# Kernel tuning notes

Measured on AMD Instinct MI355X. Metric: run time of the kernel, lower is better.

Reference implementation:

```python
import jax, jax.numpy as jnp
import numpy as np

B, N_NODES, VOCAB, H = 128, 1023, 2048, 256  # depth-9 perfect binary trees (heap layout)


def setup_inputs() -> dict:
    key = jax.random.key(0)
    k1, k2, k3, k4, k5 = jax.random.split(key, 5)
    tokens = jax.random.randint(k1, (B, N_NODES), 0, VOCAB)
    emb = jax.random.normal(k2, (VOCAB, H), dtype=jnp.float32) * 0.02
    Wx = jax.random.normal(k3, (H, 5 * H), dtype=jnp.float32) * 0.02
    Ul = jax.random.normal(k4, (H, 5 * H), dtype=jnp.float32) * 0.02
    Ur = jax.random.normal(k5, (H, 5 * H), dtype=jnp.float32) * 0.02
    b = jnp.zeros((5 * H,), dtype=jnp.float32)
    return {"tokens": tokens, "emb": emb, "Wx": Wx, "Ul": Ul, "Ur": Ur, "b": b}


def _tree_lstm(tokens, emb, Wx, Ul, Ur, b):
    # tokens: [B, 2^(D+1)-1] in level-order heap layout; children of heap index i
    # are 2i+1, 2i+2 -> within level d+1 they sit at offsets 2k, 2k+1.
    n_nodes = tokens.shape[1]
    depth = int(np.log2(n_nodes + 1)) - 1
    hdim = emb.shape[1]
    x_all = emb[tokens]  # [B, N, H] embedding lookup (memory-bound gather)
    h = c = None
    for d in range(depth, -1, -1):  # bottom-up over levels (fixed structural loop)
        start, n = 2 ** d - 1, 2 ** d
        x = x_all[:, start:start + n]  # [B, n, H]
        gates = jnp.einsum('bnh,hg->bng', x, Wx) + b
        if h is not None:
            hl, hr = h[:, 0::2], h[:, 1::2]
            cl, cr = c[:, 0::2], c[:, 1::2]
            gates = gates + jnp.einsum('bnh,hg->bng', hl, Ul) + jnp.einsum('bnh,hg->bng', hr, Ur)
        i, fl, fr, o, u = jnp.split(gates, 5, axis=-1)
        i, fl, fr, o = map(jax.nn.sigmoid, (i, fl, fr, o))
        u = jnp.tanh(u)
        c_new = i * u
        if c is not None:
            c_new = c_new + fl * cl + fr * cr
        c = c_new
        h = o * jnp.tanh(c)
    return h[:, 0], c[:, 0]  # root states, each [B, H]


def reference(tokens, emb, Wx, Ul, Ur, b):
    h_root, _ = _tree_lstm(tokens, emb, Wx, Ul, Ur, b)
    return h_root  # [B, H]
```

## Files before the change

kernel.cpp:

```cpp
#include <hip/hip_runtime.h>
#include <hip/hip_bf16.h>
#include <math.h>

#define B_SZ   128
#define HDIM   256
#define NG     1280
#define NNODES 1023
#define VOCAB  2048

typedef unsigned int uint32;
typedef short  short8v  __attribute__((ext_vector_type(8)));
typedef float  float4v  __attribute__((ext_vector_type(4)));

__device__ __forceinline__ float sigm(float x) {
    return 1.0f / (1.0f + __expf(-x));
}
__device__ __forceinline__ float tanh_fast(float x) {
    return 2.0f / (1.0f + __expf(-2.0f * x)) - 1.0f;
}
__device__ __forceinline__ float bf2f(unsigned short u) {
    return __uint_as_float(((uint32)u) << 16);
}
__device__ __forceinline__ unsigned short f2bf(float f) {
    uint32 x = __float_as_uint(f);
    uint32 r = (x + 0x7FFFu + ((x >> 16) & 1u)) >> 16;
    return (unsigned short)r;
}

__device__ __forceinline__ void dma16(const unsigned short* gptr, unsigned short* lptr) {
    __builtin_amdgcn_global_load_lds(
        (const __attribute__((address_space(1))) void*)gptr,
        (__attribute__((address_space(3))) void*)lptr, 16, 0, 0);
}

__global__ __launch_bounds__(256) void embb_kernel(
    const float* __restrict__ emb, unsigned short* __restrict__ embb)
{
    const int t = blockIdx.x * 256 + threadIdx.x;
    const float4 v0 = *(const float4*)(emb + (size_t)t * 8);
    const float4 v1 = *(const float4*)(emb + (size_t)t * 8 + 4);
    short8v o;
    o[0] = (short)f2bf(v0.x); o[1] = (short)f2bf(v0.y);
    o[2] = (short)f2bf(v0.z); o[3] = (short)f2bf(v0.w);
    o[4] = (short)f2bf(v1.x); o[5] = (short)f2bf(v1.y);
    o[6] = (short)f2bf(v1.z); o[7] = (short)f2bf(v1.w);
    *(short8v*)(embb + (size_t)t * 8) = o;
}

__global__ __launch_bounds__(256) void prep_wtf(
    const float* __restrict__ Ul, const float* __restrict__ Ur,
    const float* __restrict__ Wx, unsigned short* __restrict__ WTf)
{
    const int t = blockIdx.x * 256 + threadIdx.x;
    const int l = t & 63;
    const int q = l >> 4, c = l & 15;
    const int ks = (t >> 6) % 24;
    const int ng = t / (24 * 64);
    const int col = ng * 16 + c;
    const int k = ks * 32 + q * 8;
    const float* src = (k < 256) ? (Ul + (size_t)k * NG + col)
                     : (k < 512) ? (Ur + (size_t)(k - 256) * NG + col)
                                 : (Wx + (size_t)(k - 512) * NG + col);
    short8v v;
    #pragma unroll
    for (int j = 0; j < 8; ++j) v[j] = (short)f2bf(src[(size_t)j * NG]);
    *(short8v*)(WTf + (size_t)t * 8) = v;
}

__global__ __launch_bounds__(256, 2) void ewb_mfma(
    const unsigned short* __restrict__ WTf, const unsigned short* __restrict__ embb,
    const float* __restrict__ bias, unsigned short* __restrict__ EWb)
{
    __shared__ __align__(16) unsigned short Ab[2][4096];
    __shared__ __align__(16) unsigned short wbE[20480];

    const int tid  = threadIdx.x;
    const int lane = tid & 63;
    const int w    = tid >> 6;
    const int quad = lane >> 4, col15 = lane & 15;
    const int jt = blockIdx.x;
    const int rowBase = blockIdx.y * 64;
    const int jbase   = jt * 64;

    const unsigned short* agp[2];
    unsigned short* ldst[2];
    #pragma unroll
    for (int t = 0; t < 2; ++t) {
        const int ch = 2 * w + t, sub = ch >> 2, rt = ch & 3;
        const int srow = rowBase + rt * 16 + col15;
        agp[t]  = embb + (size_t)srow * HDIM + sub * 32 + quad * 8;
        ldst[t] = &Ab[0][0] + ch * 512;
    }

    const short8v* WTfv = (const short8v*)WTf;
    uint32 boff[5];
    #pragma unroll
    for (int g = 0; g < 5; ++g)
        boff[g] = ((g * 16 + jt * 4 + w) * 24 + 16) * 64 + lane;

    float4v acc[4][5];
    #pragma unroll
    for (int rt = 0; rt < 4; ++rt)
        #pragma unroll
        for (int g = 0; g < 5; ++g)
            #pragma unroll
            for (int e = 0; e < 4; ++e) acc[rt][g][e] = 0.0f;

    dma16(agp[0], ldst[0]); dma16(agp[1], ldst[1]);
    __syncthreads();

    #pragma unroll
    for (int s = 0; s < 4; ++s) {
        if (s < 3) {
            dma16(agp[0] + (s + 1) * 64, ldst[0] + ((s + 1) & 1) * 4096);
            dma16(agp[1] + (s + 1) * 64, ldst[1] + ((s + 1) & 1) * 4096);
        }
        #pragma unroll
        for (int sub = 0; sub < 2; ++sub) {
            short8v bf[5];
            #pragma unroll
            for (int g = 0; g < 5; ++g) bf[g] = WTfv[boff[g] + (s * 2 + sub) * 64];
            #pragma unroll
            for (int rt = 0; rt < 4; ++rt) {
                const short8v af = *(const short8v*)&Ab[s & 1][(sub * 4 + rt) * 512 + lane * 8];
                #pragma unroll
                for (int g = 0; g < 5; ++g)
                    acc[rt][g] = __builtin_amdgcn_mfma_f32_16x16x32_bf16(
                        af, bf[g], acc[rt][g], 0, 0, 0);
            }
        }
        __syncthreads();
    }

    const int jl = w * 16 + col15;
    const int j  = jbase + jl;
    float bz[5];
    #pragma unroll
    for (int g = 0; g < 5; ++g) bz[g] = bias[g * 256 + j];
    const int jchunk = jl >> 3, jpos = jl & 7;

    #pragma unroll
    for (int rt = 0; rt < 4; ++rt) {
        #pragma unroll
        for (int reg = 0; reg < 4; ++reg) {
            const int rr = rt * 16 + quad * 4 + reg;
            const int roff = ((jchunk + 2 * quad) & 7) * 8 + jpos;
            #pragma unroll
            for (int g = 0; g < 5; ++g)
                wbE[(g * 64 + rr) * 64 + roff] = f2bf(acc[rt][g][reg] + bz[g]);
        }
    }
    __syncthreads();

    #pragma unroll
    for (int k2 = 0; k2 < 10; ++k2) {
        const int c = tid + k2 * 256;
        const int g = c >> 9, rr = (c >> 3) & 63, u = c & 7;
        const int ru = (u + 2 * ((rr >> 2) & 3)) & 7;
        const short8v v = *(const short8v*)&wbE[(g * 64 + rr) * 64 + ru * 8];
        *(short8v*)(EWb + (size_t)(rowBase + rr) * NG + g * 256 + jbase + u * 8) = v;
    }
}

__global__ __launch_bounds__(256) void leaftab_kernel(
    const unsigned short* __restrict__ EWb,
    unsigned short* __restrict__ Hleaf, unsigned short* __restrict__ Cleaf)
{
    const int t = blockIdx.x * 256 + threadIdx.x;
    const int tok = t >> 8, j = t & 255;
    const float gi = bf2f(EWb[(size_t)tok * NG + j]);
    const float go = bf2f(EWb[(size_t)tok * NG + 768 + j]);
    const float gu = bf2f(EWb[(size_t)tok * NG + 1024 + j]);
    const float c = sigm(gi) * tanh_fast(gu);
    const float h = sigm(go) * tanh_fast(c);
    Hleaf[t] = f2bf(h);
    Cleaf[t] = f2bf(c);
}

__global__ __launch_bounds__(256, 2) void level_kernel(
    const unsigned short* __restrict__ WTf, const unsigned short* __restrict__ EWb,
    const int* __restrict__ tokens,
    const unsigned short* __restrict__ Hleaf, const unsigned short* __restrict__ Cleaf,
    const unsigned short* __restrict__ hsrc, const unsigned short* __restrict__ csrc,
    unsigned short* __restrict__ hdst, unsigned short* __restrict__ cdst,
    float* __restrict__ out, const int d)
{
    const int n = 1 << d;

    __shared__ __align__(16) unsigned short Ab[2][4096];
    __shared__ __align__(16) unsigned short ews[2560 * 8];
    __shared__ __align__(16) unsigned short cst[1024 * 8];

    const int tid  = threadIdx.x;
    const int lane = tid & 63;
    const int w    = tid >> 6;
    const int quad = lane >> 4, col15 = lane & 15;
    const int jt = blockIdx.x;
    const int rowBase = blockIdx.y * 64;
    const int jbase   = jt * 64;

    const unsigned short* agp_lo[2];
    const unsigned short* agp_hi[2];
    unsigned short* ldst[2];
    #pragma unroll
    for (int t = 0; t < 2; ++t) {
        const int ch = 2 * w + t, sub = ch >> 2, rt = ch & 3;
        const int srow = rowBase + rt * 16 + col15;
        if (d == 8) {
            const int b = srow >> 8, i = srow & 255;
            const int tokL = tokens[b * NNODES + 511 + 2 * i];
            const int tokR = tokens[b * NNODES + 512 + 2 * i];
            agp_lo[t] = Hleaf + (size_t)tokL * HDIM + sub * 32 + quad * 8;
            agp_hi[t] = Hleaf + (size_t)tokR * HDIM + sub * 32 + quad * 8;
        } else {
            agp_lo[t] = hsrc + (size_t)(2 * srow) * HDIM + sub * 32 + quad * 8;
            agp_hi[t] = agp_lo[t] + HDIM;
        }
        ldst[t] = &Ab[0][0] + ch * 512;
    }

    const short8v* WTfv = (const short8v*)WTf;
    uint32 boff[5];
    #pragma unroll
    for (int g = 0; g < 5; ++g)
        boff[g] = ((g * 16 + jt * 4 + w) * 24) * 64 + lane;

    float4v acc[4][5];
    #pragma unroll
    for (int rt = 0; rt < 4; ++rt)
        #pragma unroll
        for (int g = 0; g < 5; ++g)
            #pragma unroll
            for (int e = 0; e < 4; ++e) acc[rt][g][e] = 0.0f;

    dma16(agp_lo[0], ldst[0]); dma16(agp_lo[1], ldst[1]);
    __syncthreads();

    #pragma unroll
    for (int s = 0; s < 8; ++s) {
        if (s < 7) {
            const int sn = s + 1;
            #pragma unroll
            for (int t = 0; t < 2; ++t) {
                const unsigned short* p = (sn < 4) ? (agp_lo[t] + sn * 64)
                                                   : (agp_hi[t] + (sn - 4) * 64);
                dma16(p, ldst[t] + (sn & 1) * 4096);
            }
        }

        if (s >= 2 && s <= 6) {
            #pragma unroll
            for (int t2 = 0; t2 < 2; ++t2) {
                const int it = (s - 2) * 2 + t2;
                const int c = tid + it * 256;
                const uint32 row = (uint32)c / 40u;
                const int rem = c - (int)row * 40;
                const int g = rem >> 3, u = rem & 7;
                const int grow = rowBase + (int)row;
                const int tok = tokens[(grow >> d) * NNODES + (n - 1) + (grow & (n - 1))];
                dma16(EWb + (size_t)tok * NG + g * 256 + jbase + u * 8,
                      ews + ((size_t)it * 256 + w * 64) * 8);
            }
            if (s >= 5) {
                #pragma unroll
                for (int t2 = 0; t2 < 2; ++t2) {
                    const int k2 = (s - 5) * 2 + t2;
                    const int c = tid + k2 * 256;
                    const int rr = c >> 4, side = (c >> 3) & 1, u = c & 7;
                    const unsigned short* src;
                    if (d == 8) {
                        const int grow = rowBase + rr;
                        const int b = grow >> 8, i = grow & 255;
                        const int tok = tokens[b * NNODES + 511 + 2 * i + side];
                        src = Cleaf + (size_t)tok * HDIM + jbase + u * 8;
                    } else {
                        src = csrc + (size_t)(2 * (rowBase + rr) + side) * HDIM + jbase + u * 8;
                    }
                    dma16(src, cst + ((size_t)k2 * 256 + w * 64) * 8);
                }
            }
        }

        #pragma unroll
        for (int sub = 0; sub < 2; ++sub) {
            short8v bf[5];
            #pragma unroll
            for (int g = 0; g < 5; ++g) bf[g] = WTfv[boff[g] + (s * 2 + sub) * 64];
            #pragma unroll
            for (int rt = 0; rt < 4; ++rt) {
                const short8v af = *(const short8v*)&Ab[s & 1][(sub * 4 + rt) * 512 + lane * 8];
                #pragma unroll
                for (int g = 0; g < 5; ++g)
                    acc[rt][g] = __builtin_amdgcn_mfma_f32_16x16x32_bf16(
                        af, bf[g], acc[rt][g], 0, 0, 0);
            }
        }
        __syncthreads();
    }

    const int jl = w * 16 + col15;
    const int j  = jbase + jl;
    float hv[4][4], cv[4][4];
    #pragma unroll
    for (int rt = 0; rt < 4; ++rt) {
        #pragma unroll
        for (int reg = 0; reg < 4; ++reg) {
            const int rr = rt * 16 + quad * 4 + reg;
            const float gi  = acc[rt][0][reg] + bf2f(ews[rr * 320 +       jl]);
            const float gfl = acc[rt][1][reg] + bf2f(ews[rr * 320 +  64 + jl]);
            const float gfr = acc[rt][2][reg] + bf2f(ews[rr * 320 + 128 + jl]);
            const float go  = acc[rt][3][reg] + bf2f(ews[rr * 320 + 192 + jl]);
            const float gu  = acc[rt][4][reg] + bf2f(ews[rr * 320 + 256 + jl]);
            const float cl  = bf2f(cst[rr * 128 +      jl]);
            const float cr  = bf2f(cst[rr * 128 + 64 + jl]);
            const float ii = sigm(gi), fl = sigm(gfl), fr = sigm(gfr), oo = sigm(go);
            const float uu = tanh_fast(gu);
            const float c = ii * uu + fl * cl + fr * cr;
            const float h = oo * tanh_fast(c);
            cv[rt][reg] = c; hv[rt][reg] = h;
            if (d == 0) out[(size_t)(rowBase + rr) * HDIM + j] = h;
        }
    }
    __syncthreads();

    const int jchunk = jl >> 3, jpos = jl & 7;
    #pragma unroll
    for (int rt = 0; rt < 4; ++rt) {
        #pragma unroll
        for (int reg = 0; reg < 4; ++reg) {
            const int rr = rt * 16 + quad * 4 + reg;
            const int roff = ((jchunk + 2 * quad) & 7) * 8 + jpos;
            ews[rr * 64 + roff]        = f2bf(hv[rt][reg]);
            ews[4096 + rr * 64 + roff] = f2bf(cv[rt][reg]);
        }
    }
    __syncthreads();
    #pragma unroll
    for (int k2 = 0; k2 < 4; ++k2) {
        const int c = tid + k2 * 256;
        const int arr = c >> 9, rr = (c >> 3) & 63, u = c & 7;
        const int ru = (u + 2 * ((rr >> 2) & 3)) & 7;
        const short8v v = *(const short8v*)(ews + (arr * 4096 + rr * 64 + ru * 8));
        unsigned short* dstp = (arr ? cdst : hdst) +
            (size_t)(rowBase + rr) * HDIM + jbase + u * 8;
        *(short8v*)dstp = v;
    }
}

extern "C" void kernel_launch(void* const* d_in, const int* in_sizes, int n_in,
                              void* d_out, int out_size, void* d_ws, size_t ws_size,
                              hipStream_t stream)
{
    const int*   tokens = (const int*)d_in[0];
    const float* emb    = (const float*)d_in[1];
    const float* Wx     = (const float*)d_in[2];
    const float* Ul     = (const float*)d_in[3];
    const float* Ur     = (const float*)d_in[4];
    const float* bias   = (const float*)d_in[5];
    float* out = (float*)d_out;

    const size_t EW_ELEMS  = (size_t)VOCAB * NG;
    const size_t EMB_ELEMS = (size_t)VOCAB * HDIM;
    const size_t WTF_ELEMS = (size_t)80 * 24 * 64 * 8;
    const size_t LT_ELEMS  = (size_t)VOCAB * HDIM;
    const size_t SLOT_A    = (size_t)16384 * HDIM;
    const size_t SLOT_B    = (size_t)32768 * HDIM;
    const size_t REQUIRED  = (EW_ELEMS + EMB_ELEMS + WTF_ELEMS + 2 * LT_ELEMS
                              + 2 * (SLOT_A + SLOT_B)) * 2;
    if (ws_size < REQUIRED || d_ws == nullptr) return;

    char* ws = (char*)d_ws;
    unsigned short* EWb   = (unsigned short*)ws;
    unsigned short* embb  = EWb + EW_ELEMS;
    unsigned short* WTf   = embb + EMB_ELEMS;
    unsigned short* Hleaf = WTf + WTF_ELEMS;
    unsigned short* Cleaf = Hleaf + LT_ELEMS;
    unsigned short* hA    = Cleaf + LT_ELEMS;
    unsigned short* cA    = hA + SLOT_A;
    unsigned short* hB    = cA + SLOT_A;
    unsigned short* cB    = hB + SLOT_B;

    embb_kernel<<<dim3(256), 256, 0, stream>>>(emb, embb);
    prep_wtf<<<dim3(480), 256, 0, stream>>>(Ul, Ur, Wx, WTf);
    ewb_mfma<<<dim3(4, 32), 256, 0, stream>>>(WTf, embb, bias, EWb);
    leaftab_kernel<<<dim3(2048), 256, 0, stream>>>(EWb, Hleaf, Cleaf);

    for (int d = 8; d >= 0; --d) {
        const int NRB = 2 << d;
        const bool evenD = ((d & 1) == 0);
        const unsigned short* hs = evenD ? hA : hB;
        const unsigned short* cs = evenD ? cA : cB;
        unsigned short* hd = evenD ? hB : hA;
        unsigned short* cd = evenD ? cB : cA;
        level_kernel<<<dim3(4, NRB), 256, 0, stream>>>(
            WTf, EWb, tokens, Hleaf, Cleaf, hs, cs, hd, cd, out, d);
    }
}
```

Before: 340.8 us.

## Drop LDS staging of gate/cell inputs, read them directly in epilogue, raise occupancy

Removes the shared-memory buffers that staged the precomputed embedding-gate rows and child cell states through async copies during the GEMM loop. The epilogue now loads these values straight from global memory per element and reuses the A-tile LDS buffer for the output transpose. LDS drops to 16 KB, so launch bounds go to 4 blocks per SIMD-group for higher occupancy. The trade-off is that the global loads are no longer overlapped with the MFMA loop, and the per-element 2-byte scattered reads are uncoalesced. The tighter register budget may also cause spills.

Result: slower. 448.4 us (+31.5%).

```diff
diff --git a/kernel.cpp b/kernel.cpp
--- a/kernel.cpp
+++ b/kernel.cpp
@@ -177,7 +177,7 @@
     Cleaf[t] = f2bf(c);
 }
 
-__global__ __launch_bounds__(256, 2) void level_kernel(
+__global__ __launch_bounds__(256, 4) void level_kernel(
     const unsigned short* __restrict__ WTf, const unsigned short* __restrict__ EWb,
     const int* __restrict__ tokens,
     const unsigned short* __restrict__ Hleaf, const unsigned short* __restrict__ Cleaf,
@@ -188,8 +188,6 @@
     const int n = 1 << d;
 
     __shared__ __align__(16) unsigned short Ab[2][4096];
-    __shared__ __align__(16) unsigned short ews[2560 * 8];
-    __shared__ __align__(16) unsigned short cst[1024 * 8];
 
     const int tid  = threadIdx.x;
     const int lane = tid & 63;
@@ -248,39 +246,6 @@
             }
         }
 
-        if (s >= 2 && s <= 6) {
-            #pragma unroll
-            for (int t2 = 0; t2 < 2; ++t2) {
-                const int it = (s - 2) * 2 + t2;
-                const int c = tid + it * 256;
-                const uint32 row = (uint32)c / 40u;
-                const int rem = c - (int)row * 40;
-                const int g = rem >> 3, u = rem & 7;
-                const int grow = rowBase + (int)row;
-                const int tok = tokens[(grow >> d) * NNODES + (n - 1) + (grow & (n - 1))];
-                dma16(EWb + (size_t)tok * NG + g * 256 + jbase + u * 8,
-                      ews + ((size_t)it * 256 + w * 64) * 8);
-            }
-            if (s >= 5) {
-                #pragma unroll
-                for (int t2 = 0; t2 < 2; ++t2) {
-                    const int k2 = (s - 5) * 2 + t2;
-                    const int c = tid + k2 * 256;
-                    const int rr = c >> 4, side = (c >> 3) & 1, u = c & 7;
-                    const unsigned short* src;
-                    if (d == 8) {
-                        const int grow = rowBase + rr;
-                        const int b = grow >> 8, i = grow & 255;
-                        const int tok = tokens[b * NNODES + 511 + 2 * i + side];
-                        src = Cleaf + (size_t)tok * HDIM + jbase + u * 8;
-                    } else {
-                        src = csrc + (size_t)(2 * (rowBase + rr) + side) * HDIM + jbase + u * 8;
-                    }
-                    dma16(src, cst + ((size_t)k2 * 256 + w * 64) * 8);
-                }
-            }
-        }
-
         #pragma unroll
         for (int sub = 0; sub < 2; ++sub) {
             short8v bf[5];
@@ -306,23 +271,36 @@
         #pragma unroll
         for (int reg = 0; reg < 4; ++reg) {
             const int rr = rt * 16 + quad * 4 + reg;
-            const float gi  = acc[rt][0][reg] + bf2f(ews[rr * 320 +       jl]);
-            const float gfl = acc[rt][1][reg] + bf2f(ews[rr * 320 +  64 + jl]);
-            const float gfr = acc[rt][2][reg] + bf2f(ews[rr * 320 + 128 + jl]);
-            const float go  = acc[rt][3][reg] + bf2f(ews[rr * 320 + 192 + jl]);
-            const float gu  = acc[rt][4][reg] + bf2f(ews[rr * 320 + 256 + jl]);
-            const float cl  = bf2f(cst[rr * 128 +      jl]);
-            const float cr  = bf2f(cst[rr * 128 + 64 + jl]);
+            const int grow = rowBase + rr;
+            const int tok = tokens[(grow >> d) * NNODES + (n - 1) + (grow & (n - 1))];
+            const unsigned short* ewp = EWb + (size_t)tok * NG + j;
+            float cl, cr;
+            if (d == 8) {
+                const int b = grow >> 8, i = grow & 255;
+                const int tokL = tokens[b * NNODES + 511 + 2 * i];
+                const int tokR = tokens[b * NNODES + 512 + 2 * i];
+                cl = bf2f(Cleaf[(size_t)tokL * HDIM + j]);
+                cr = bf2f(Cleaf[(size_t)tokR * HDIM + j]);
+            } else {
+                cl = bf2f(csrc[(size_t)(2 * grow) * HDIM + j]);
+                cr = bf2f(csrc[(size_t)(2 * grow + 1) * HDIM + j]);
+            }
+            const float gi  = acc[rt][0][reg] + bf2f(ewp[0]);
+            const float gfl = acc[rt][1][reg] + bf2f(ewp[256]);
+            const float gfr = acc[rt][2][reg] + bf2f(ewp[512]);
+            const float go  = acc[rt][3][reg] + bf2f(ewp[768]);
+            const float gu  = acc[rt][4][reg] + bf2f(ewp[1024]);
             const float ii = sigm(gi), fl = sigm(gfl), fr = sigm(gfr), oo = sigm(go);
             const float uu = tanh_fast(gu);
             const float c = ii * uu + fl * cl + fr * cr;
             const float h = oo * tanh_fast(c);
             cv[rt][reg] = c; hv[rt][reg] = h;
-            if (d == 0) out[(size_t)(rowBase + rr) * HDIM + j] = h;
-        }
-    }
-    __syncthreads();
-
+            if (d == 0) out[(size_t)grow * HDIM + j] = h;
+        }
+    }
+    if (d == 0) return;
+
+    unsigned short* wb = &Ab[0][0];
     const int jchunk = jl >> 3, jpos = jl & 7;
     #pragma unroll
     for (int rt = 0; rt < 4; ++rt) {
@@ -330,8 +308,8 @@
         for (int reg = 0; reg < 4; ++reg) {
             const int rr = rt * 16 + quad * 4 + reg;
             const int roff = ((jchunk + 2 * quad) & 7) * 8 + jpos;
-            ews[rr * 64 + roff]        = f2bf(hv[rt][reg]);
-            ews[4096 + rr * 64 + roff] = f2bf(cv[rt][reg]);
+            wb[rr * 64 + roff]        = f2bf(hv[rt][reg]);
+            wb[4096 + rr * 64 + roff] = f2bf(cv[rt][reg]);
         }
     }
     __syncthreads();
@@ -340,7 +318,7 @@
         const int c = tid + k2 * 256;
         const int arr = c >> 9, rr = (c >> 3) & 63, u = c & 7;
         const int ru = (u + 2 * ((rr >> 2) & 3)) & 7;
-        const short8v v = *(const short8v*)(ews + (arr * 4096 + rr * 64 + ru * 8));
+        const short8v v = *(const short8v*)(wb + (arr * 4096 + rr * 64 + ru * 8));
         unsigned short* dstp = (arr ? cdst : hdst) +
             (size_t)(rowBase + rr) * HDIM + jbase + u * 8;
         *(short8v*)dstp = v;
```
